# Performance work log

Measured on AMD Instinct MI355X. Metric: run time of the kernel, lower is better.

Reference implementation:

```python
import jax, jax.numpy as jnp
import numpy as np

SUBSTEP = 10
FRAMES = 24
T = FRAMES * SUBSTEP
DT = 1.0 / 60.0 / SUBSTEP
SLOPE_DEG = 20.0
COS_S = float(np.cos(np.deg2rad(SLOPE_DEG)))
SIN_S = float(np.sin(np.deg2rad(SLOPE_DEG)))
INIT_HEIGHT = 0.1
N_VERTS = 2_000_000
GRAVITY = jnp.array([0.0, -9.8, 0.0], dtype=jnp.float32)
CONTACT_N = jnp.array([-SIN_S, COS_S, 0.0], dtype=jnp.float32)
EPS = 1e-6


def quat_mul(a, b):
    w1, x1, y1, z1 = a[0], a[1], a[2], a[3]
    w2, x2, y2, z2 = b[0], b[1], b[2], b[3]
    return jnp.stack([
        w1 * w2 - x1 * x2 - y1 * y2 - z1 * z2,
        w1 * x2 + x1 * w2 + y1 * z2 - z1 * y2,
        w1 * y2 + y1 * w2 + z1 * x2 - x1 * z2,
        w1 * z2 + z1 * w2 + x1 * y2 - y1 * x2,
    ])


def quat_to_matrix(q):
    q = q / jnp.linalg.norm(q)
    w, x, y, z = q[0], q[1], q[2], q[3]
    return jnp.stack([
        jnp.stack([1 - 2 * y * y - 2 * z * z, 2 * x * y - 2 * w * z, 2 * x * z + 2 * w * y]),
        jnp.stack([2 * x * y + 2 * w * z, 1 - 2 * x * x - 2 * z * z, 2 * y * z - 2 * w * x]),
        jnp.stack([2 * x * z - 2 * w * y, 2 * y * z + 2 * w * x, 1 - 2 * x * x - 2 * y * y]),
    ])


def cross_matrix(a):
    z = jnp.zeros((), dtype=a.dtype)
    return jnp.stack([
        jnp.stack([z, -a[2], a[1]]),
        jnp.stack([a[2], z, -a[0]]),
        jnp.stack([-a[1], a[0], z]),
    ])


def setup_inputs() -> dict:
    key = jax.random.key(0)
    k1, k2, k3 = jax.random.split(key, 3)
    return {
        "x": jax.random.normal(k1, (N_VERTS, 3), dtype=jnp.float32) * 0.2,
        "mass_center": jnp.zeros((3,), dtype=jnp.float32),
        "init_trans": jax.random.normal(k2, (3,), dtype=jnp.float32) * 0.3 + jnp.array([0.3, 0.5, 0.0]),
        "init_quat": jnp.ones((4,), dtype=jnp.float32),
        "init_v": jax.random.normal(k3, (3,), dtype=jnp.float32) * 0.1,
        "kn": jnp.array([0.5], dtype=jnp.float32),
        "mu": jnp.array([0.4], dtype=jnp.float32),
        "linear_damping": jnp.array([0.999], dtype=jnp.float32),
        "angular_damping": jnp.array([0.998], dtype=jnp.float32),
    }


def _simulate(x, mass_center, init_trans, init_quat, init_v, kn, mu, linear_damping, angular_damping):
    n = x.shape[0]
    mass = jnp.asarray(float(n), dtype=x.dtype)  # unit mass per vertex
    inv_mass = 1.0 / mass
    r = x - mass_center
    # inertia_reference = sum_i m*( (r.r) I - outer(r,r) )
    inertia = jnp.sum(jnp.einsum('ni,ni->n', r, r)) * jnp.eye(3, dtype=x.dtype) - jnp.einsum('ni,nj->ij', r, r)
    kn0, mu0 = kn[0], mu[0]
    ld, ad = linear_damping[0], angular_damping[0]
    eye3 = jnp.eye(3, dtype=x.dtype)

    def step(carry, _):
        trans, quat, v, omega = carry
        Rm = quat_to_matrix(quat)
        Rx = x @ Rm.T                                   # [N,3]
        xi = trans + Rx + mass_center                   # world positions
        vi_all = v + jnp.cross(omega[None, :], Rx)      # per-vertex velocities
        d = xi @ CONTACT_N
        rel_v = vi_all @ CONTACT_N
        mask = (d < -COS_S * INIT_HEIGHT) & (rel_v < 0.0)
        num = jnp.sum(mask)
        numf = jnp.maximum(num, 1).astype(x.dtype)
        sum_pos = jnp.sum(x * mask[:, None].astype(x.dtype), axis=0)
        ri = sum_pos / numf
        Ri = Rm @ ri
        vi = v + jnp.cross(omega, Ri)
        v_n = jnp.dot(vi, CONTACT_N) * CONTACT_N
        v_t = vi - v_n
        vn_new = -kn0 * v_n
        alpha = jnp.maximum(1.0 - mu0 * (1.0 + kn0) * (jnp.linalg.norm(v_n) / (jnp.linalg.norm(v_t) + EPS)), 0.0)
        vi_new = vn_new + alpha * v_t
        I = Rm @ inertia @ Rm.T
        I_inv = jnp.linalg.inv(I)
        Rri = cross_matrix(Ri)
        kmat = inv_mass * eye3 - Rri @ I_inv @ Rri
        J = jnp.linalg.solve(kmat, vi_new - vi)
        hit = num > 0
        dv = jnp.where(hit, J * inv_mass, 0.0)
        domega = jnp.where(hit, I_inv @ Rri @ J, 0.0)
        v_new = (v + GRAVITY * DT) * ld + dv
        omega_new = omega * ad + domega
        trans_new = trans + DT * v_new
        wq = jnp.concatenate([jnp.zeros((1,), dtype=x.dtype), omega_new]) * (0.5 * DT)
        quat_new = quat + quat_mul(wq, quat)
        quat_new = quat_new / jnp.linalg.norm(quat_new)
        new_carry = (trans_new, quat_new, v_new, omega_new)
        return new_carry, jnp.concatenate([trans_new, quat_new])

    carry0 = (init_trans, init_quat / jnp.linalg.norm(init_quat), init_v, jnp.zeros(3, dtype=x.dtype))
    _, traj = jax.lax.scan(step, carry0, None, length=T)
    return traj  # [T, 7] = translation(3) + quaternion(4) per substep


def reference(x, mass_center, init_trans, init_quat, init_v, kn, mu, linear_damping, angular_damping):
    return _simulate(x, mass_center, init_trans, init_quat, init_v, kn, mu, linear_damping, angular_damping)
```

## Files before the change

### kernel.cpp

```cpp
#include <hip/hip_runtime.h>

#define GRID    256
#define BLOCK   512
#define NWAVES  (BLOCK / 64)
#define CHUNK   7813

typedef unsigned long long u64;

__device__ __forceinline__ u64 rec_load(const u64* p) {
  return __hip_atomic_load(p, __ATOMIC_RELAXED, __HIP_MEMORY_SCOPE_AGENT);
}
__device__ __forceinline__ void rec_store(u64* p, u64 v) {
  __hip_atomic_store(p, v, __ATOMIC_RELAXED, __HIP_MEMORY_SCOPE_AGENT);
}
__device__ __forceinline__ u64 rec_pack(float f, unsigned tag) {
  return (u64)__float_as_uint(f) | ((u64)tag << 32);
}

template <int NV>
__device__ __forceinline__ void block_reduce(float* v, float* sm) {
  #pragma unroll
  for (int off = 32; off > 0; off >>= 1) {
    #pragma unroll
    for (int k = 0; k < NV; ++k) v[k] += __shfl_down(v[k], off, 64);
  }
  const int lane = threadIdx.x & 63;
  const int wid  = threadIdx.x >> 6;
  if (lane == 0) {
    #pragma unroll
    for (int k = 0; k < NV; ++k) sm[wid * NV + k] = v[k];
  }
  __syncthreads();
  if (threadIdx.x == 0) {
    #pragma unroll
    for (int w = 1; w < NWAVES; ++w) {
      #pragma unroll
      for (int k = 0; k < NV; ++k) v[k] += sm[w * NV + k];
    }
  }
  __syncthreads();
}

__device__ __forceinline__ void mat3_mul(const float* A, const float* B, float* C) {
  #pragma unroll
  for (int i = 0; i < 3; ++i)
    #pragma unroll
    for (int j = 0; j < 3; ++j)
      C[i*3+j] = A[i*3+0]*B[0*3+j] + A[i*3+1]*B[1*3+j] + A[i*3+2]*B[2*3+j];
}
__device__ __forceinline__ void mat3_mul_bt(const float* A, const float* B, float* C) {
  #pragma unroll
  for (int i = 0; i < 3; ++i)
    #pragma unroll
    for (int j = 0; j < 3; ++j)
      C[i*3+j] = A[i*3+0]*B[j*3+0] + A[i*3+1]*B[j*3+1] + A[i*3+2]*B[j*3+2];
}
__device__ __forceinline__ void mat3_inv(const float* m, float* inv) {
  float A =  (m[4]*m[8] - m[5]*m[7]);
  float B = -(m[3]*m[8] - m[5]*m[6]);
  float C =  (m[3]*m[7] - m[4]*m[6]);
  float det = m[0]*A + m[1]*B + m[2]*C;
  float id = 1.0f / det;
  inv[0] = A * id;
  inv[1] = -(m[1]*m[8] - m[2]*m[7]) * id;
  inv[2] =  (m[1]*m[5] - m[2]*m[4]) * id;
  inv[3] = B * id;
  inv[4] =  (m[0]*m[8] - m[2]*m[6]) * id;
  inv[5] = -(m[0]*m[5] - m[2]*m[3]) * id;
  inv[6] = C * id;
  inv[7] = -(m[0]*m[7] - m[1]*m[6]) * id;
  inv[8] =  (m[0]*m[4] - m[1]*m[3]) * id;
}

__global__ __launch_bounds__(BLOCK)
void sim_kernel(const float* __restrict__ xg,
                const float* __restrict__ mc_p,
                const float* __restrict__ itr_p,
                const float* __restrict__ iq_p,
                const float* __restrict__ iv_p,
                const float* __restrict__ kn_p,
                const float* __restrict__ mu_p,
                const float* __restrict__ ldp_p,
                const float* __restrict__ adp_p,
                float* __restrict__ out,
                u64* __restrict__ ws,
                int N, int T)
{
  const int tid = threadIdx.x;
  const int bid = blockIdx.x;

  extern __shared__ float dyn[];
  float* sXx = dyn;
  float* sXy = dyn + CHUNK;
  float* sXz = dyn + 2 * CHUNK;
  __shared__ float s_red[NWAVES * 8];
  __shared__ float s_plane[8];

  const float nx  = (float)(-0.3420201433256687);
  const float ny  = (float)( 0.9396926207859084);
  const float DTF = (float)(1.0 / 60.0 / 10.0);
  const float HDT = (float)(0.5 * (1.0 / 60.0 / 10.0));
  const float DTH = (float)(-0.9396926207859084 * 0.1);
  const float GYDT = -9.8f * (float)(1.0 / 60.0 / 10.0);

  const float mc0 = mc_p[0], mc1 = mc_p[1], mc2 = mc_p[2];

  u64* part0 = ws;
  u64* part1 = ws + 4 * GRID;
  u64* st    = ws + 8 * GRID;
  u64* bufI  = ws + 8 * GRID + 128;

  const int vstart = bid * CHUNK;
  int cl = N - vstart; if (cl > CHUNK) cl = CHUNK; if (cl < 0) cl = 0;

  for (int i = tid; i < cl; i += BLOCK) {
    const float* p = xg + (size_t)(vstart + i) * 3;
    sXx[i] = p[0]; sXy[i] = p[1]; sXz[i] = p[2];
  }
  __syncthreads();

  {
    float v6[6] = {0,0,0,0,0,0};
    for (int i = tid; i < cl; i += BLOCK) {
      float r0 = sXx[i] - mc0, r1 = sXy[i] - mc1, r2 = sXz[i] - mc2;
      v6[0] += r0*r0; v6[1] += r1*r1; v6[2] += r2*r2;
      v6[3] += r0*r1; v6[4] += r0*r2; v6[5] += r1*r2;
    }
    block_reduce<6>(v6, s_red);
    if (tid == 0) {
      #pragma unroll
      for (int k = 0; k < 6; ++k) rec_store(bufI + k * GRID + bid, rec_pack(v6[k], 0xC0FFEEu));
    }
  }

  float In[9];
  if (bid == 0) {
    float v6[6] = {0,0,0,0,0,0};
    if (tid < GRID) {
      u64 r[6];
      int f = 0;
      for (;;) {
        #pragma unroll
        for (int k = 0; k < 6; ++k) r[k] = rec_load(bufI + k * GRID + tid);
        bool ok = true;
        #pragma unroll
        for (int k = 0; k < 6; ++k) ok &= ((unsigned)(r[k] >> 32) == 0xC0FFEEu);
        if (ok) break;
        if ((++f & 15) == 0) __builtin_amdgcn_s_sleep(1);
      }
      #pragma unroll
      for (int k = 0; k < 6; ++k) v6[k] = __uint_as_float((unsigned)r[k]);
    }
    block_reduce<6>(v6, s_red);
    float trc = v6[0] + v6[1] + v6[2];
    In[0] = trc - v6[0]; In[4] = trc - v6[1]; In[8] = trc - v6[2];
    In[1] = -v6[3]; In[3] = -v6[3];
    In[2] = -v6[4]; In[6] = -v6[4];
    In[5] = -v6[5]; In[7] = -v6[5];
  }

  float tr0 = itr_p[0], tr1 = itr_p[1], tr2 = itr_p[2];
  float q0 = iq_p[0], q1 = iq_p[1], q2 = iq_p[2], q3 = iq_p[3];
  {
    float n0 = sqrtf(q0*q0 + q1*q1 + q2*q2 + q3*q3);
    q0 /= n0; q1 /= n0; q2 /= n0; q3 /= n0;
  }
  float v0 = iv_p[0], v1 = iv_p[1], v2 = iv_p[2];
  float om0 = 0.f, om1 = 0.f, om2 = 0.f;
  const float knv = kn_p[0], muv = mu_p[0], ldv = ldp_p[0], adv = adp_p[0];
  const float inv_mass = 1.0f / (float)N;

  float Rm[9];

  if (tid == 0) {
    float qn = sqrtf(q0*q0 + q1*q1 + q2*q2 + q3*q3);
    float w = q0/qn, xq = q1/qn, yq = q2/qn, zq = q3/qn;
    Rm[0] = 1.f - 2.f*yq*yq - 2.f*zq*zq; Rm[1] = 2.f*xq*yq - 2.f*w*zq; Rm[2] = 2.f*xq*zq + 2.f*w*yq;
    Rm[3] = 2.f*xq*yq + 2.f*w*zq; Rm[4] = 1.f - 2.f*xq*xq - 2.f*zq*zq; Rm[5] = 2.f*yq*zq - 2.f*w*xq;
    Rm[6] = 2.f*xq*zq - 2.f*w*yq; Rm[7] = 2.f*yq*zq + 2.f*w*xq; Rm[8] = 1.f - 2.f*xq*xq - 2.f*yq*yq;
    float a0 = Rm[0]*nx + Rm[3]*ny;
    float a1 = Rm[1]*nx + Rm[4]*ny;
    float a2 = Rm[2]*nx + Rm[5]*ny;
    float w0 = ny*om2, w1 = -nx*om2, w2 = nx*om1 - ny*om0;
    float b0 = Rm[0]*w0 + Rm[3]*w1 + Rm[6]*w2;
    float b1 = Rm[1]*w0 + Rm[4]*w1 + Rm[7]*w2;
    float b2 = Rm[2]*w0 + Rm[5]*w1 + Rm[8]*w2;
    float ca = DTH - ((tr0 + mc0)*nx + (tr1 + mc1)*ny);
    float cb = -(v0*nx + v1*ny);
    s_plane[0] = a0; s_plane[1] = a1; s_plane[2] = a2;
    s_plane[3] = b0; s_plane[4] = b1; s_plane[5] = b2;
    s_plane[6] = ca; s_plane[7] = cb;
  }
  __syncthreads();

  for (int t = 0; t < T; ++t) {
    const float a0 = s_plane[0], a1 = s_plane[1], a2 = s_plane[2];
    const float b0 = s_plane[3], b1 = s_plane[4], b2 = s_plane[5];
    const float ca = s_plane[6], cb = s_plane[7];

    float acc[4] = {0.f, 0.f, 0.f, 0.f};
    for (int i = tid; i < cl; i += BLOCK) {
      float x0 = sXx[i], x1 = sXy[i], x2 = sXz[i];
      float da = x0*a0 + x1*a1 + x2*a2;
      float db = x0*b0 + x1*b1 + x2*b2;
      if (da < ca && db < cb) { acc[0] += 1.f; acc[1] += x0; acc[2] += x1; acc[3] += x2; }
    }
    block_reduce<4>(acc, s_red);

    const unsigned want = (unsigned)(t + 1);
    u64* pb = (t & 1) ? part1 : part0;
    if (tid == 0) {
      #pragma unroll
      for (int k = 0; k < 4; ++k) rec_store(pb + k * GRID + bid, rec_pack(acc[k], want));
    }

    if (bid == 0) {
      float tot[4] = {0.f, 0.f, 0.f, 0.f};
      if (tid < GRID) {
        u64 r0, r1, r2, r3;
        int f = 0;
        for (;;) {
          r0 = rec_load(pb + 0 * GRID + tid);
          r1 = rec_load(pb + 1 * GRID + tid);
          r2 = rec_load(pb + 2 * GRID + tid);
          r3 = rec_load(pb + 3 * GRID + tid);
          if ((unsigned)(r0 >> 32) == want && (unsigned)(r1 >> 32) == want &&
              (unsigned)(r2 >> 32) == want && (unsigned)(r3 >> 32) == want) break;
          if ((++f & 15) == 0) __builtin_amdgcn_s_sleep(1);
        }
        tot[0] = __uint_as_float((unsigned)r0);
        tot[1] = __uint_as_float((unsigned)r1);
        tot[2] = __uint_as_float((unsigned)r2);
        tot[3] = __uint_as_float((unsigned)r3);
      }
      block_reduce<4>(tot, s_red);

      if (tid == 0) {
        float num = tot[0];
        float numf = fmaxf(num, 1.0f);
        float ri0 = tot[1] / numf, ri1 = tot[2] / numf, ri2 = tot[3] / numf;
        float Ri0 = Rm[0]*ri0 + Rm[1]*ri1 + Rm[2]*ri2;
        float Ri1 = Rm[3]*ri0 + Rm[4]*ri1 + Rm[5]*ri2;
        float Ri2 = Rm[6]*ri0 + Rm[7]*ri1 + Rm[8]*ri2;
        float dv0 = 0.f, dv1 = 0.f, dv2 = 0.f, dm0 = 0.f, dm1 = 0.f, dm2 = 0.f;
        if (num > 0.0f) {
          float vi0 = v0 + om1*Ri2 - om2*Ri1;
          float vi1 = v1 + om2*Ri0 - om0*Ri2;
          float vi2 = v2 + om0*Ri1 - om1*Ri0;
          float vdn = vi0*nx + vi1*ny;
          float vn0 = vdn*nx, vn1 = vdn*ny;
          float vt0 = vi0 - vn0, vt1 = vi1 - vn1, vt2 = vi2;
          float nvn = sqrtf(vn0*vn0 + vn1*vn1);
          float nvt = sqrtf(vt0*vt0 + vt1*vt1 + vt2*vt2);
          float alpha = fmaxf(1.0f - muv*(1.0f + knv)*(nvn/(nvt + 1e-6f)), 0.0f);
          float dvi0 = (-knv*vn0 + alpha*vt0) - vi0;
          float dvi1 = (-knv*vn1 + alpha*vt1) - vi1;
          float dvi2 = (alpha*vt2) - vi2;
          float Tm[9]; mat3_mul(Rm, In, Tm);
          float Iw[9]; mat3_mul_bt(Tm, Rm, Iw);
          float Ii[9]; mat3_inv(Iw, Ii);
          float Cx[9] = {0.f, -Ri2, Ri1,  Ri2, 0.f, -Ri0,  -Ri1, Ri0, 0.f};
          float T2[9]; mat3_mul(Cx, Ii, T2);
          float T3[9]; mat3_mul(T2, Cx, T3);
          float K[9];
          #pragma unroll
          for (int k = 0; k < 9; ++k) K[k] = -T3[k];
          K[0] += inv_mass; K[4] += inv_mass; K[8] += inv_mass;
          float Ki[9]; mat3_inv(K, Ki);
          float J0 = Ki[0]*dvi0 + Ki[1]*dvi1 + Ki[2]*dvi2;
          float J1 = Ki[3]*dvi0 + Ki[4]*dvi1 + Ki[5]*dvi2;
          float J2 = Ki[6]*dvi0 + Ki[7]*dvi1 + Ki[8]*dvi2;
          dv0 = J0*inv_mass; dv1 = J1*inv_mass; dv2 = J2*inv_mass;
          float c0 = -Ri2*J1 + Ri1*J2;
          float c1 =  Ri2*J0 - Ri0*J2;
          float c2 = -Ri1*J0 + Ri0*J1;
          dm0 = Ii[0]*c0 + Ii[1]*c1 + Ii[2]*c2;
          dm1 = Ii[3]*c0 + Ii[4]*c1 + Ii[5]*c2;
          dm2 = Ii[6]*c0 + Ii[7]*c1 + Ii[8]*c2;
        }
        v0 = v0*ldv + dv0;
        v1 = (v1 + GYDT)*ldv + dv1;
        v2 = v2*ldv + dv2;
        om0 = om0*adv + dm0; om1 = om1*adv + dm1; om2 = om2*adv + dm2;
        tr0 = tr0 + DTF*v0; tr1 = tr1 + DTF*v1; tr2 = tr2 + DTF*v2;
        float wx = om0*HDT, wy = om1*HDT, wz = om2*HDT;
        float dq0 = -wx*q1 - wy*q2 - wz*q3;
        float dq1 =  wx*q0 + wy*q3 - wz*q2;
        float dq2 =  wy*q0 + wz*q1 - wx*q3;
        float dq3 =  wz*q0 + wx*q2 - wy*q1;
        q0 += dq0; q1 += dq1; q2 += dq2; q3 += dq3;
        float qn2 = sqrtf(q0*q0 + q1*q1 + q2*q2 + q3*q3);
        q0 /= qn2; q1 /= qn2; q2 /= qn2; q3 /= qn2;
        float* o = out + (size_t)t * 7;
        o[0] = tr0; o[1] = tr1; o[2] = tr2;
        o[3] = q0;  o[4] = q1;  o[5] = q2;  o[6] = q3;
        float qn = sqrtf(q0*q0 + q1*q1 + q2*q2 + q3*q3);
        float w = q0/qn, xq = q1/qn, yq = q2/qn, zq = q3/qn;
        Rm[0] = 1.f - 2.f*yq*yq - 2.f*zq*zq; Rm[1] = 2.f*xq*yq - 2.f*w*zq; Rm[2] = 2.f*xq*zq + 2.f*w*yq;
        Rm[3] = 2.f*xq*yq + 2.f*w*zq; Rm[4] = 1.f - 2.f*xq*xq - 2.f*zq*zq; Rm[5] = 2.f*yq*zq - 2.f*w*xq;
        Rm[6] = 2.f*xq*zq - 2.f*w*yq; Rm[7] = 2.f*yq*zq + 2.f*w*xq; Rm[8] = 1.f - 2.f*xq*xq - 2.f*yq*yq;
        float na0 = Rm[0]*nx + Rm[3]*ny;
        float na1 = Rm[1]*nx + Rm[4]*ny;
        float na2 = Rm[2]*nx + Rm[5]*ny;
        float w0 = ny*om2, w1 = -nx*om2, w2 = nx*om1 - ny*om0;
        float nb0 = Rm[0]*w0 + Rm[3]*w1 + Rm[6]*w2;
        float nb1 = Rm[1]*w0 + Rm[4]*w1 + Rm[7]*w2;
        float nb2 = Rm[2]*w0 + Rm[5]*w1 + Rm[8]*w2;
        float nca = DTH - ((tr0 + mc0)*nx + (tr1 + mc1)*ny);
        float ncb = -(v0*nx + v1*ny);
        s_plane[0] = na0; s_plane[1] = na1; s_plane[2] = na2;
        s_plane[3] = nb0; s_plane[4] = nb1; s_plane[5] = nb2;
        s_plane[6] = nca; s_plane[7] = ncb;
      }
      __syncthreads();
      if (tid < 64) {
        u64* sl = st + (size_t)((t + 1) & 1) * 64;
        rec_store(sl + tid, rec_pack(s_plane[tid & 7], want));
      }
    } else {
      if (tid < 8) {
        const u64* sl = st + (size_t)((t + 1) & 1) * 64 + (size_t)(bid & 7) * 8;
        u64 r; int f = 0;
        for (;;) {
          r = rec_load(sl + tid);
          if ((unsigned)(r >> 32) == want) break;
          if ((++f & 31) == 0) __builtin_amdgcn_s_sleep(1);
        }
        s_plane[tid] = __uint_as_float((unsigned)r);
      }
      __syncthreads();
    }
  }
}

extern "C" void kernel_launch(void* const* d_in, const int* in_sizes, int n_in,
                              void* d_out, int out_size, void* d_ws, size_t ws_size,
                              hipStream_t stream) {
  const float* x   = (const float*)d_in[0];
  const float* mc  = (const float*)d_in[1];
  const float* itr = (const float*)d_in[2];
  const float* iq  = (const float*)d_in[3];
  const float* iv  = (const float*)d_in[4];
  const float* kn  = (const float*)d_in[5];
  const float* mu  = (const float*)d_in[6];
  const float* ldp = (const float*)d_in[7];
  const float* adp = (const float*)d_in[8];
  float* out = (float*)d_out;
  u64* ws  = (u64*)d_ws;
  int N = in_sizes[0] / 3;
  int T = out_size / 7;

  const int dyn_lds = 3 * CHUNK * 4;
  hipFuncSetAttribute((const void*)sim_kernel,
                      hipFuncAttributeMaxDynamicSharedMemorySize, dyn_lds);

  void* args[] = {(void*)&x, (void*)&mc, (void*)&itr, (void*)&iq, (void*)&iv,
                  (void*)&kn, (void*)&mu, (void*)&ldp, (void*)&adp,
                  (void*)&out, (void*)&ws, (void*)&N, (void*)&T};
  hipLaunchCooperativeKernel((void*)sim_kernel, dim3(GRID), dim3(BLOCK),
                             args, dyn_lds, stream);
}
```

Before: 1.583 ms.

## Restructure per-step grid sync: split master/worker loops, wave-parallel polling, off-critical-path inertia

Splits the timestep loop into separate paths for block 0 and the worker blocks. Workers now poll the plane record with a whole wave and a ballot, then broadcast it by shuffle instead of going through shared memory and a block barrier. Block 0 reads all partials with 512 threads at two loads each instead of 256 threads at four. It also writes the plane records directly from thread 0 and moves the world-inertia inverse and the output writes after the publish, so they leave the critical path between steps. The aim is lower per-step synchronisation latency across the 240 sequential steps, at the cost of more complex workspace indexing that assumes GRID=256.

```diff
diff --git a/kernel.cpp b/kernel.cpp
--- a/kernel.cpp
+++ b/kernel.cpp
@@ -86,14 +86,18 @@
                 u64* __restrict__ ws,
                 int N, int T)
 {
-  const int tid = threadIdx.x;
-  const int bid = blockIdx.x;
+  const int tid  = threadIdx.x;
+  const int bid  = blockIdx.x;
+  const int lane = tid & 63;
+  const int wid  = tid >> 6;
 
   extern __shared__ float dyn[];
   float* sXx = dyn;
   float* sXy = dyn + CHUNK;
   float* sXz = dyn + 2 * CHUNK;
-  __shared__ float s_red[NWAVES * 8];
+  __shared__ float s_red6[NWAVES * 6];
+  __shared__ float s_red4[NWAVES * 4];
+  __shared__ float s_red2[NWAVES * 2];
   __shared__ float s_plane[8];
 
   const float nx  = (float)(-0.3420201433256687);
@@ -106,9 +110,9 @@
   const float mc0 = mc_p[0], mc1 = mc_p[1], mc2 = mc_p[2];
 
   u64* part0 = ws;
-  u64* part1 = ws + 4 * GRID;
-  u64* st    = ws + 8 * GRID;
-  u64* bufI  = ws + 8 * GRID + 128;
+  u64* part1 = ws + 1024;
+  u64* st    = ws + 2048;
+  u64* bufI  = ws + 2176;
 
   const int vstart = bid * CHUNK;
   int cl = N - vstart; if (cl > CHUNK) cl = CHUNK; if (cl < 0) cl = 0;
@@ -126,7 +130,7 @@
       v6[0] += r0*r0; v6[1] += r1*r1; v6[2] += r2*r2;
       v6[3] += r0*r1; v6[4] += r0*r2; v6[5] += r1*r2;
     }
-    block_reduce<6>(v6, s_red);
+    block_reduce<6>(v6, s_red6);
     if (tid == 0) {
       #pragma unroll
       for (int k = 0; k < 6; ++k) rec_store(bufI + k * GRID + bid, rec_pack(v6[k], 0xC0FFEEu));
@@ -151,7 +155,7 @@
       #pragma unroll
       for (int k = 0; k < 6; ++k) v6[k] = __uint_as_float((unsigned)r[k]);
     }
-    block_reduce<6>(v6, s_red);
+    block_reduce<6>(v6, s_red6);
     float trc = v6[0] + v6[1] + v6[2];
     In[0] = trc - v6[0]; In[4] = trc - v6[1]; In[8] = trc - v6[2];
     In[1] = -v6[3]; In[3] = -v6[3];
@@ -171,74 +175,98 @@
   const float inv_mass = 1.0f / (float)N;
 
   float Rm[9];
-
-  if (tid == 0) {
+  float Ii[9];
+  float a0, a1, a2, b0, b1, b2, ca, cb;
+
+  {
     float qn = sqrtf(q0*q0 + q1*q1 + q2*q2 + q3*q3);
     float w = q0/qn, xq = q1/qn, yq = q2/qn, zq = q3/qn;
-    Rm[0] = 1.f - 2.f*yq*yq - 2.f*zq*zq; Rm[1] = 2.f*xq*yq - 2.f*w*zq; Rm[2] = 2.f*xq*zq + 2.f*w*yq;
-    Rm[3] = 2.f*xq*yq + 2.f*w*zq; Rm[4] = 1.f - 2.f*xq*xq - 2.f*zq*zq; Rm[5] = 2.f*yq*zq - 2.f*w*xq;
-    Rm[6] = 2.f*xq*zq - 2.f*w*yq; Rm[7] = 2.f*yq*zq + 2.f*w*xq; Rm[8] = 1.f - 2.f*xq*xq - 2.f*yq*yq;
-    float a0 = Rm[0]*nx + Rm[3]*ny;
-    float a1 = Rm[1]*nx + Rm[4]*ny;
-    float a2 = Rm[2]*nx + Rm[5]*ny;
+    float R0 = 1.f - 2.f*yq*yq - 2.f*zq*zq, R1 = 2.f*xq*yq - 2.f*w*zq, R2 = 2.f*xq*zq + 2.f*w*yq;
+    float R3 = 2.f*xq*yq + 2.f*w*zq, R4 = 1.f - 2.f*xq*xq - 2.f*zq*zq, R5 = 2.f*yq*zq - 2.f*w*xq;
+    float R6 = 2.f*xq*zq - 2.f*w*yq, R7 = 2.f*yq*zq + 2.f*w*xq, R8 = 1.f - 2.f*xq*xq - 2.f*yq*yq;
+    a0 = R0*nx + R3*ny; a1 = R1*nx + R4*ny; a2 = R2*nx + R5*ny;
     float w0 = ny*om2, w1 = -nx*om2, w2 = nx*om1 - ny*om0;
-    float b0 = Rm[0]*w0 + Rm[3]*w1 + Rm[6]*w2;
-    float b1 = Rm[1]*w0 + Rm[4]*w1 + Rm[7]*w2;
-    float b2 = Rm[2]*w0 + Rm[5]*w1 + Rm[8]*w2;
-    float ca = DTH - ((tr0 + mc0)*nx + (tr1 + mc1)*ny);
-    float cb = -(v0*nx + v1*ny);
-    s_plane[0] = a0; s_plane[1] = a1; s_plane[2] = a2;
-    s_plane[3] = b0; s_plane[4] = b1; s_plane[5] = b2;
-    s_plane[6] = ca; s_plane[7] = cb;
-  }
-  __syncthreads();
-
-  for (int t = 0; t < T; ++t) {
-    const float a0 = s_plane[0], a1 = s_plane[1], a2 = s_plane[2];
-    const float b0 = s_plane[3], b1 = s_plane[4], b2 = s_plane[5];
-    const float ca = s_plane[6], cb = s_plane[7];
-
-    float acc[4] = {0.f, 0.f, 0.f, 0.f};
-    for (int i = tid; i < cl; i += BLOCK) {
-      float x0 = sXx[i], x1 = sXy[i], x2 = sXz[i];
-      float da = x0*a0 + x1*a1 + x2*a2;
-      float db = x0*b0 + x1*b1 + x2*b2;
-      if (da < ca && db < cb) { acc[0] += 1.f; acc[1] += x0; acc[2] += x1; acc[3] += x2; }
-    }
-    block_reduce<4>(acc, s_red);
-
-    const unsigned want = (unsigned)(t + 1);
-    u64* pb = (t & 1) ? part1 : part0;
-    if (tid == 0) {
-      #pragma unroll
-      for (int k = 0; k < 4; ++k) rec_store(pb + k * GRID + bid, rec_pack(acc[k], want));
-    }
-
-    if (bid == 0) {
-      float tot[4] = {0.f, 0.f, 0.f, 0.f};
-      if (tid < GRID) {
-        u64 r0, r1, r2, r3;
+    b0 = R0*w0 + R3*w1 + R6*w2;
+    b1 = R1*w0 + R4*w1 + R7*w2;
+    b2 = R2*w0 + R5*w1 + R8*w2;
+    ca = DTH - ((tr0 + mc0)*nx + (tr1 + mc1)*ny);
+    cb = -(v0*nx + v1*ny);
+    if (bid == 0 && tid == 0) {
+      Rm[0]=R0; Rm[1]=R1; Rm[2]=R2; Rm[3]=R3; Rm[4]=R4; Rm[5]=R5; Rm[6]=R6; Rm[7]=R7; Rm[8]=R8;
+      s_plane[0]=a0; s_plane[1]=a1; s_plane[2]=a2;
+      s_plane[3]=b0; s_plane[4]=b1; s_plane[5]=b2;
+      s_plane[6]=ca; s_plane[7]=cb;
+      float Tm[9]; mat3_mul(Rm, In, Tm);
+      float Iw[9]; mat3_mul_bt(Tm, Rm, Iw);
+      mat3_inv(Iw, Ii);
+    }
+  }
+
+  if (bid == 0) {
+    for (int t = 0; t < T; ++t) {
+      __syncthreads();
+      a0 = s_plane[0]; a1 = s_plane[1]; a2 = s_plane[2];
+      b0 = s_plane[3]; b1 = s_plane[4]; b2 = s_plane[5];
+      ca = s_plane[6]; cb = s_plane[7];
+
+      float acc[4] = {0.f, 0.f, 0.f, 0.f};
+      for (int i = tid; i < cl; i += BLOCK) {
+        float x0 = sXx[i], x1 = sXy[i], x2 = sXz[i];
+        float da = x0*a0 + x1*a1 + x2*a2;
+        float db = x0*b0 + x1*b1 + x2*b2;
+        if (da < ca && db < cb) { acc[0] += 1.f; acc[1] += x0; acc[2] += x1; acc[3] += x2; }
+      }
+      #pragma unroll
+      for (int off = 32; off > 0; off >>= 1) {
+        #pragma unroll
+        for (int k = 0; k < 4; ++k) acc[k] += __shfl_down(acc[k], off, 64);
+      }
+      if (lane == 0) {
+        #pragma unroll
+        for (int k = 0; k < 4; ++k) s_red4[wid * 4 + k] = acc[k];
+      }
+      __syncthreads();
+      const unsigned want = (unsigned)(t + 1);
+      u64* pb = (t & 1) ? part1 : part0;
+      if (tid == 0) {
+        #pragma unroll
+        for (int w = 1; w < NWAVES; ++w) {
+          #pragma unroll
+          for (int k = 0; k < 4; ++k) acc[k] += s_red4[w * 4 + k];
+        }
+        #pragma unroll
+        for (int k = 0; k < 4; ++k) rec_store(pb + k * GRID + 0, rec_pack(acc[k], want));
+      }
+
+      u64 wA, wB;
+      {
         int f = 0;
         for (;;) {
-          r0 = rec_load(pb + 0 * GRID + tid);
-          r1 = rec_load(pb + 1 * GRID + tid);
-          r2 = rec_load(pb + 2 * GRID + tid);
-          r3 = rec_load(pb + 3 * GRID + tid);
-          if ((unsigned)(r0 >> 32) == want && (unsigned)(r1 >> 32) == want &&
-              (unsigned)(r2 >> 32) == want && (unsigned)(r3 >> 32) == want) break;
+          wA = rec_load(pb + tid);
+          wB = rec_load(pb + 512 + tid);
+          if ((unsigned)(wA >> 32) == want && (unsigned)(wB >> 32) == want) break;
           if ((++f & 15) == 0) __builtin_amdgcn_s_sleep(1);
         }
-        tot[0] = __uint_as_float((unsigned)r0);
-        tot[1] = __uint_as_float((unsigned)r1);
-        tot[2] = __uint_as_float((unsigned)r2);
-        tot[3] = __uint_as_float((unsigned)r3);
-      }
-      block_reduce<4>(tot, s_red);
+      }
+      float pA = __uint_as_float((unsigned)wA);
+      float pB = __uint_as_float((unsigned)wB);
+      #pragma unroll
+      for (int off = 32; off > 0; off >>= 1) {
+        pA += __shfl_down(pA, off, 64);
+        pB += __shfl_down(pB, off, 64);
+      }
+      if (lane == 0) { s_red2[wid * 2] = pA; s_red2[wid * 2 + 1] = pB; }
+      __syncthreads();
 
       if (tid == 0) {
-        float num = tot[0];
+        float tot0 = s_red2[0] + s_red2[2]  + s_red2[4]  + s_red2[6];
+        float tot2 = s_red2[1] + s_red2[3]  + s_red2[5]  + s_red2[7];
+        float tot1 = s_red2[8] + s_red2[10] + s_red2[12] + s_red2[14];
+        float tot3 = s_red2[9] + s_red2[11] + s_red2[13] + s_red2[15];
+
+        float num = tot0;
         float numf = fmaxf(num, 1.0f);
-        float ri0 = tot[1] / numf, ri1 = tot[2] / numf, ri2 = tot[3] / numf;
+        float ri0 = tot1 / numf, ri1 = tot2 / numf, ri2 = tot3 / numf;
         float Ri0 = Rm[0]*ri0 + Rm[1]*ri1 + Rm[2]*ri2;
         float Ri1 = Rm[3]*ri0 + Rm[4]*ri1 + Rm[5]*ri2;
         float Ri2 = Rm[6]*ri0 + Rm[7]*ri1 + Rm[8]*ri2;
@@ -256,9 +284,6 @@
           float dvi0 = (-knv*vn0 + alpha*vt0) - vi0;
           float dvi1 = (-knv*vn1 + alpha*vt1) - vi1;
           float dvi2 = (alpha*vt2) - vi2;
-          float Tm[9]; mat3_mul(Rm, In, Tm);
-          float Iw[9]; mat3_mul_bt(Tm, Rm, Iw);
-          float Ii[9]; mat3_inv(Iw, Ii);
           float Cx[9] = {0.f, -Ri2, Ri1,  Ri2, 0.f, -Ri0,  -Ri1, Ri0, 0.f};
           float T2[9]; mat3_mul(Cx, Ii, T2);
           float T3[9]; mat3_mul(T2, Cx, T3);
@@ -291,44 +316,87 @@
         q0 += dq0; q1 += dq1; q2 += dq2; q3 += dq3;
         float qn2 = sqrtf(q0*q0 + q1*q1 + q2*q2 + q3*q3);
         q0 /= qn2; q1 /= qn2; q2 /= qn2; q3 /= qn2;
-        float* o = out + (size_t)t * 7;
-        o[0] = tr0; o[1] = tr1; o[2] = tr2;
-        o[3] = q0;  o[4] = q1;  o[5] = q2;  o[6] = q3;
+
         float qn = sqrtf(q0*q0 + q1*q1 + q2*q2 + q3*q3);
         float w = q0/qn, xq = q1/qn, yq = q2/qn, zq = q3/qn;
         Rm[0] = 1.f - 2.f*yq*yq - 2.f*zq*zq; Rm[1] = 2.f*xq*yq - 2.f*w*zq; Rm[2] = 2.f*xq*zq + 2.f*w*yq;
         Rm[3] = 2.f*xq*yq + 2.f*w*zq; Rm[4] = 1.f - 2.f*xq*xq - 2.f*zq*zq; Rm[5] = 2.f*yq*zq - 2.f*w*xq;
         Rm[6] = 2.f*xq*zq - 2.f*w*yq; Rm[7] = 2.f*yq*zq + 2.f*w*xq; Rm[8] = 1.f - 2.f*xq*xq - 2.f*yq*yq;
-        float na0 = Rm[0]*nx + Rm[3]*ny;
-        float na1 = Rm[1]*nx + Rm[4]*ny;
-        float na2 = Rm[2]*nx + Rm[5]*ny;
+        float pl[8];
+        pl[0] = Rm[0]*nx + Rm[3]*ny;
+        pl[1] = Rm[1]*nx + Rm[4]*ny;
+        pl[2] = Rm[2]*nx + Rm[5]*ny;
         float w0 = ny*om2, w1 = -nx*om2, w2 = nx*om1 - ny*om0;
-        float nb0 = Rm[0]*w0 + Rm[3]*w1 + Rm[6]*w2;
-        float nb1 = Rm[1]*w0 + Rm[4]*w1 + Rm[7]*w2;
-        float nb2 = Rm[2]*w0 + Rm[5]*w1 + Rm[8]*w2;
-        float nca = DTH - ((tr0 + mc0)*nx + (tr1 + mc1)*ny);
-        float ncb = -(v0*nx + v1*ny);
-        s_plane[0] = na0; s_plane[1] = na1; s_plane[2] = na2;
-        s_plane[3] = nb0; s_plane[4] = nb1; s_plane[5] = nb2;
-        s_plane[6] = nca; s_plane[7] = ncb;
+        pl[3] = Rm[0]*w0 + Rm[3]*w1 + Rm[6]*w2;
+        pl[4] = Rm[1]*w0 + Rm[4]*w1 + Rm[7]*w2;
+        pl[5] = Rm[2]*w0 + Rm[5]*w1 + Rm[8]*w2;
+        pl[6] = DTH - ((tr0 + mc0)*nx + (tr1 + mc1)*ny);
+        pl[7] = -(v0*nx + v1*ny);
+
+        u64* sl = st + (size_t)((t + 1) & 1) * 64;
+        #pragma unroll
+        for (int r = 0; r < 8; ++r) {
+          #pragma unroll
+          for (int k = 0; k < 8; ++k) rec_store(sl + r * 8 + k, rec_pack(pl[k], want));
+        }
+        #pragma unroll
+        for (int k = 0; k < 8; ++k) s_plane[k] = pl[k];
+        float* o = out + (size_t)t * 7;
+        o[0] = tr0; o[1] = tr1; o[2] = tr2;
+        o[3] = q0;  o[4] = q1;  o[5] = q2;  o[6] = q3;
+        float Tm[9]; mat3_mul(Rm, In, Tm);
+        float Iw[9]; mat3_mul_bt(Tm, Rm, Iw);
+        mat3_inv(Iw, Ii);
+      }
+    }
+  } else {
+    const int rep = bid & 7;
+    for (int t = 0; t < T; ++t) {
+      if (t > 0) {
+        const u64* sl = st + (size_t)(t & 1) * 64 + (size_t)rep * 8;
+        u64 v;
+        int f = 0;
+        for (;;) {
+          v = rec_load(sl + (lane & 7));
+          bool ok = ((unsigned)(v >> 32) == (unsigned)t);
+          unsigned long long m = __ballot(ok);
+          if ((m & 0xFFull) == 0xFFull) break;
+          if ((++f & 7) == 0) __builtin_amdgcn_s_sleep(1);
+        }
+        float fv = __uint_as_float((unsigned)v);
+        a0 = __shfl(fv, 0, 64); a1 = __shfl(fv, 1, 64); a2 = __shfl(fv, 2, 64);
+        b0 = __shfl(fv, 3, 64); b1 = __shfl(fv, 4, 64); b2 = __shfl(fv, 5, 64);
+        ca = __shfl(fv, 6, 64); cb = __shfl(fv, 7, 64);
+      }
+
+      float acc[4] = {0.f, 0.f, 0.f, 0.f};
+      for (int i = tid; i < cl; i += BLOCK) {
+        float x0 = sXx[i], x1 = sXy[i], x2 = sXz[i];
+        float da = x0*a0 + x1*a1 + x2*a2;
+        float db = x0*b0 + x1*b1 + x2*b2;
+        if (da < ca && db < cb) { acc[0] += 1.f; acc[1] += x0; acc[2] += x1; acc[3] += x2; }
+      }
+      #pragma unroll
+      for (int off = 32; off > 0; off >>= 1) {
+        #pragma unroll
+        for (int k = 0; k < 4; ++k) acc[k] += __shfl_down(acc[k], off, 64);
+      }
+      if (lane == 0) {
+        #pragma unroll
+        for (int k = 0; k < 4; ++k) s_red4[wid * 4 + k] = acc[k];
       }
       __syncthreads();
-      if (tid < 64) {
-        u64* sl = st + (size_t)((t + 1) & 1) * 64;
-        rec_store(sl + tid, rec_pack(s_plane[tid & 7], want));
-      }
-    } else {
-      if (tid < 8) {
-        const u64* sl = st + (size_t)((t + 1) & 1) * 64 + (size_t)(bid & 7) * 8;
-        u64 r; int f = 0;
-        for (;;) {
-          r = rec_load(sl + tid);
-          if ((unsigned)(r >> 32) == want) break;
-          if ((++f & 31) == 0) __builtin_amdgcn_s_sleep(1);
-        }
-        s_plane[tid] = __uint_as_float((unsigned)r);
-      }
-      __syncthreads();
+      if (tid == 0) {
+        #pragma unroll
+        for (int w = 1; w < NWAVES; ++w) {
+          #pragma unroll
+          for (int k = 0; k < 4; ++k) acc[k] += s_red4[w * 4 + k];
+        }
+        const unsigned want = (unsigned)(t + 1);
+        u64* pb = (t & 1) ? part1 : part0;
+        #pragma unroll
+        for (int k = 0; k < 4; ++k) rec_store(pb + k * GRID + bid, rec_pack(acc[k], want));
+      }
     }
   }
 }
```

After: 1.834 ms. 1.16x slower.
